# Kernel optimization log

Measured on AMD Instinct MI355X. Metric: run time of the kernel, lower is better.

The kernel has to match this reference:

```python
import jax, jax.numpy as jnp
import numpy as np
from jax import lax

D_MODEL = 512
EXPAND = 2
INNER = D_MODEL * EXPAND
K = 4
B, T = 8, 2048
LN_EPS = 1e-5


def setup_inputs() -> dict:
    key = jax.random.key(0)
    ks = jax.random.split(key, 12)
    s_in = 1.0 / np.sqrt(D_MODEL)
    s_out = 1.0 / np.sqrt(INNER)
    return {
        "x": jax.random.normal(ks[0], (B, T, D_MODEL), dtype=jnp.float32),
        "ln_w": jnp.ones((D_MODEL,), jnp.float32),
        "ln_b": jnp.zeros((D_MODEL,), jnp.float32),
        "in_proj_w": jax.random.uniform(ks[1], (3 * INNER, D_MODEL), jnp.float32, -s_in, s_in),
        "in_proj_b": jax.random.uniform(ks[2], (3 * INNER,), jnp.float32, -s_in, s_in),
        "conv_w": jax.random.uniform(ks[3], (INNER, 1, K), jnp.float32, -0.5, 0.5),
        "conv_b": jax.random.uniform(ks[4], (INNER,), jnp.float32, -0.5, 0.5),
        "delta_w": jax.random.uniform(ks[5], (INNER, D_MODEL), jnp.float32, -s_in, s_in),
        "delta_b": jax.random.uniform(ks[6], (INNER,), jnp.float32, -s_in, s_in),
        "state_mix": jnp.zeros((INNER,), jnp.float32),
        "skip_scale": jnp.ones((INNER,), jnp.float32),
        "out_proj_w": jax.random.uniform(ks[7], (D_MODEL, INNER), jnp.float32, -s_out, s_out),
        "out_proj_b": jax.random.uniform(ks[8], (D_MODEL,), jnp.float32, -s_out, s_out),
    }


def _layernorm(x, w, b):
    mu = jnp.mean(x, axis=-1, keepdims=True)
    var = jnp.mean(jnp.square(x - mu), axis=-1, keepdims=True)
    return (x - mu) * lax.rsqrt(var + LN_EPS) * w + b


def _causal_dw_conv(x_bct, w, b):
    # x: [B, C, T], w: [C, 1, K] depthwise, left pad K-1 (causal)
    y = lax.conv_general_dilated(
        x_bct, w, window_strides=(1,), padding=[(K - 1, 0)],
        dimension_numbers=("NCH", "OIH", "NCH"), feature_group_count=INNER)
    return y + b[None, :, None]


def reference(x, ln_w, ln_b, in_proj_w, in_proj_b, conv_w, conv_b,
              delta_w, delta_b, state_mix, skip_scale, out_proj_w, out_proj_b):
    residual = x
    xn = _layernorm(x, ln_w, ln_b)                      # [B,T,D]
    h = xn @ in_proj_w.T + in_proj_b                     # [B,T,3*INNER]
    proj, gate, drive = jnp.split(h, 3, axis=-1)
    proj = jax.nn.silu(proj)
    gate = jax.nn.sigmoid(gate)
    conv_out = _causal_dw_conv(jnp.swapaxes(proj, 1, 2), conv_w, conv_b)
    conv_out = jnp.swapaxes(conv_out, 1, 2)              # [B,T,INNER]
    delta = jnp.maximum(jax.nn.sigmoid(xn @ delta_w.T + delta_b), 1e-4)
    drive = jnp.tanh(drive)
    a = jax.nn.sigmoid(state_mix)                        # [INNER]
    d = delta * drive                                    # [B,T,INNER]

    def step(state, d_t):
        state = a * state + d_t
        return state, state

    _, states = lax.scan(step, jnp.zeros((x.shape[0], INNER), x.dtype),
                         jnp.swapaxes(d, 0, 1))          # [T,B,INNER]
    states = jnp.swapaxes(states, 0, 1)                  # [B,T,INNER]
    y = (states + skip_scale * conv_out) * gate
    y = y @ out_proj_w.T + out_proj_b
    return residual + y
```

## Files before the change

### kernel.cpp

```cpp
#include <hip/hip_runtime.h>
#include <stdint.h>

#define D_MODEL 512
#define INNER   1024
#define NCAT    4096
#define BATCH   8
#define SEQ     2048
#define ROWS    (BATCH*SEQ)
#define LN_EPS  1e-5f
#define CHUNK   64
#define NCHUNK  (SEQ/CHUNK)

typedef unsigned short u16;
typedef unsigned int   u32;
typedef __attribute__((ext_vector_type(8))) short bf16x8;
typedef __attribute__((ext_vector_type(4))) float f32x4;

__device__ __forceinline__ u16 f2bf(float f) {
  u32 u = __builtin_bit_cast(u32, f);
  return (u16)((u + 0x7FFFu + ((u >> 16) & 1u)) >> 16);
}
__device__ __forceinline__ float bf2f(u32 lo) {
  return __builtin_bit_cast(float, lo << 16);
}
__device__ __forceinline__ float sigf(float x){ return 1.f/(1.f+__expf(-x)); }

__device__ __forceinline__ void glds16(const void* g, void* l) {
  __builtin_amdgcn_global_load_lds((const __attribute__((address_space(1))) void*)g,
                                   (__attribute__((address_space(3))) void*)l, 16, 0, 0);
}

#define MFMA16(a,b,c) __builtin_amdgcn_mfma_f32_16x16x32_bf16((a),(b),(c),0,0,0)

__global__ __launch_bounds__(256) void prep_kernel(const float* __restrict__ x,
    const float* __restrict__ lw, const float* __restrict__ lb,
    const float* __restrict__ ipw, const float* __restrict__ dw,
    const float* __restrict__ opw, const float* __restrict__ ipb,
    const float* __restrict__ db, u16* __restrict__ xn,
    u16* __restrict__ wcat, u16* __restrict__ wout, float* __restrict__ bcat) {
  const int bid = blockIdx.x;
  if (bid < ROWS/4) {
    const int row  = bid * 4 + (threadIdx.x >> 6);
    const int lane = threadIdx.x & 63;
    const float4* xr = (const float4*)(x + (size_t)row * D_MODEL);
    float4 v0 = xr[lane*2], v1 = xr[lane*2+1];
    float s  = v0.x+v0.y+v0.z+v0.w + v1.x+v1.y+v1.z+v1.w;
    float s2 = v0.x*v0.x+v0.y*v0.y+v0.z*v0.z+v0.w*v0.w
             + v1.x*v1.x+v1.y*v1.y+v1.z*v1.z+v1.w*v1.w;
    #pragma unroll
    for (int o=32;o;o>>=1){ s += __shfl_xor(s,o); s2 += __shfl_xor(s2,o); }
    const float mu = s * (1.f/D_MODEL);
    const float rs = rsqrtf(s2*(1.f/D_MODEL) - mu*mu + LN_EPS);
    const float4* wv = (const float4*)lw; const float4* bv = (const float4*)lb;
    float4 w0 = wv[lane*2], w1 = wv[lane*2+1];
    float4 b0 = bv[lane*2], b1 = bv[lane*2+1];
    u32 p0 = (u32)f2bf((v0.x-mu)*rs*w0.x+b0.x) | ((u32)f2bf((v0.y-mu)*rs*w0.y+b0.y)<<16);
    u32 p1 = (u32)f2bf((v0.z-mu)*rs*w0.z+b0.z) | ((u32)f2bf((v0.w-mu)*rs*w0.w+b0.w)<<16);
    u32 p2 = (u32)f2bf((v1.x-mu)*rs*w1.x+b1.x) | ((u32)f2bf((v1.y-mu)*rs*w1.y+b1.y)<<16);
    u32 p3 = (u32)f2bf((v1.z-mu)*rs*w1.z+b1.z) | ((u32)f2bf((v1.w-mu)*rs*w1.w+b1.w)<<16);
    ((uint4*)(xn + (size_t)row * D_MODEL))[lane] = make_uint4(p0,p1,p2,p3);
  } else {
    const int i = (bid - ROWS/4)*256 + threadIdx.x;
    const int NW1 = NCAT*D_MODEL, NW2 = D_MODEL*INNER, STR = 1024*256;
    for (int idx = i; idx < NW1; idx += STR) {
      const int r = idx >> 9, c = idx & 511;
      float v;
      if (r < 2048) v = ipw[idx];
      else {
        const int rr = r - 2048;
        v = (rr & 1) ? dw[(size_t)(rr>>1)*D_MODEL + c]
                     : ipw[(size_t)(2048 + (rr>>1))*D_MODEL + c];
      }
      wcat[idx] = f2bf(v);
    }
    for (int idx = i; idx < NW2; idx += STR) wout[idx] = f2bf(opw[idx]);
    if (i < NCAT) {
      float b;
      if (i < 2048) b = ipb[i];
      else { const int rr = i - 2048; b = (rr & 1) ? db[rr>>1] : ipb[2048 + (rr>>1)]; }
      bcat[i] = b;
    }
  }
}

__device__ __forceinline__ void sched_blk(int nbm, int nbn, int GM, int GN,
                                          int& bM, int& bN) {
  const int nwg = nbm * nbn;
  const int bid = blockIdx.x;
  const int cpx = nwg >> 3;
  const int swz = (bid & 7) * cpx + (bid >> 3);
  const int gsz = GM * GN;
  const int g   = swz / gsz, loc = swz - g * gsz;
  const int ngn = nbn / GN;
  const int gm  = g / ngn,  gn  = g - gm * ngn;
  bM = gm * GM + (loc % GM);
  bN = gn * GN + (loc / GM);
}

__global__ __launch_bounds__(512, 2) void gemm1_kernel(const u16* __restrict__ A,
    const u16* __restrict__ Bm, const float* __restrict__ bcat,
    const float* __restrict__ sm, u16* __restrict__ proj, u16* __restrict__ gate,
    u16* __restrict__ dbuf, float* __restrict__ cS) {
  extern __shared__ u16 lds[];
  const int tid = threadIdx.x;
  int bM, bN; sched_blk(ROWS/256, NCAT/256, 8, 4, bM, bN);

  const u16* gA0; const u16* gA1; const u16* gB0; const u16* gB1;
  {
    const int p0 = tid,        q0 = p0>>3, t0 = (p0&7) ^ (q0&7);
    const int p1 = 512 + tid,  q1 = p1>>3, t1 = (p1&7) ^ (q1&7);
    const int rA0 = q0*2 + (t0>>2), sA0 = t0&3;
    const int rA1 = q1*2 + (t1>>2), sA1 = t1&3;
    gA0 = A + (size_t)(bM*256 + rA0)*D_MODEL + sA0*8;
    gA1 = A + (size_t)(bM*256 + rA1)*D_MODEL + sA1*8;
    const int c0 = (rA0 & ~63) + ((rA0&15)*4) + ((rA0>>4)&3);
    const int c1 = (rA1 & ~63) + ((rA1&15)*4) + ((rA1>>4)&3);
    gB0 = Bm + (size_t)(bN*256 + c0)*D_MODEL + sA0*8;
    gB1 = Bm + (size_t)(bN*256 + c1)*D_MODEL + sA1*8;
  }

#define STAGE1(KOFF, BUFO) do { \
    glds16(gA0 + (KOFF), lds + (BUFO) + tid*8); \
    glds16(gA1 + (KOFF), lds + (BUFO) + 4096 + tid*8); \
    glds16(gB0 + (KOFF), lds + (BUFO) + 8192 + tid*8); \
    glds16(gB1 + (KOFF), lds + (BUFO) + 12288 + tid*8); } while(0)

  const int lane = tid & 63, wid = tid >> 6;
  const int wm = wid >> 2, wn = wid & 3;
  const int rl = lane & 15;
  const int e  = (((lane&1)<<2) + (lane>>4)) ^ (rl>>1);
  const int aoff = wm*4096 + (rl>>1)*64 + e*8;
  const int boff = 8192 + wn*2048 + (rl>>1)*64 + e*8;

  f32x4 acc[8][4];
  #pragma unroll
  for (int m=0;m<8;m++)
    #pragma unroll
    for (int n=0;n<4;n++) acc[m][n] = (f32x4){0.f,0.f,0.f,0.f};

  STAGE1(0, 0);
  STAGE1(32, 16384);
  asm volatile("s_waitcnt vmcnt(4)" ::: "memory");
  __builtin_amdgcn_s_barrier();
  __builtin_amdgcn_sched_barrier(0);

  int cur = 0, stg = 32768;
  for (int kt = 0; kt < 16; ++kt) {
    bf16x8 af[8], bfr[4];
    #pragma unroll
    for (int m=0;m<8;m++) af[m]  = *(const bf16x8*)&lds[cur + aoff + m*512];
    #pragma unroll
    for (int n=0;n<4;n++) bfr[n] = *(const bf16x8*)&lds[cur + boff + n*512];
    if (kt + 2 < 16) STAGE1((kt+2)*32, stg);
    #pragma unroll
    for (int m=0;m<8;m++)
      #pragma unroll
      for (int n=0;n<4;n++)
        acc[m][n] = MFMA16(af[m], bfr[n], acc[m][n]);
    if (kt + 2 < 16) { asm volatile("s_waitcnt vmcnt(4)" ::: "memory"); }
    else             { asm volatile("s_waitcnt vmcnt(0)" ::: "memory"); }
    __builtin_amdgcn_s_barrier();
    __builtin_amdgcn_sched_barrier(0);
    cur += 16384; if (cur == 49152) cur = 0;
    stg += 16384; if (stg == 49152) stg = 0;
  }
#undef STAGE1

  const int colb = bN*256 + wn*64 + rl*4;
  const float4 b4 = *(const float4*)&bcat[colb];
  const float* bp = (const float*)&b4;
  if (colb < 2048) {
    u16* outp = (colb < 1024) ? proj : gate;
    const int lcolb = colb & (INNER-1);
    #pragma unroll
    for (int m=0;m<8;m++) {
      const int row0 = bM*256 + wm*128 + m*16 + ((lane>>4)<<2);
      #pragma unroll
      for (int r=0;r<4;r++) {
        float a4[4];
        #pragma unroll
        for (int n=0;n<4;n++) {
          float v = acc[m][n][r] + bp[n];
          a4[n] = (colb < 1024) ? v * sigf(v) : sigf(v);
        }
        u32 lo = (u32)f2bf(a4[0]) | ((u32)f2bf(a4[1])<<16);
        u32 hi = (u32)f2bf(a4[2]) | ((u32)f2bf(a4[3])<<16);
        *(uint2*)&outp[(size_t)(row0+r)*INNER + lcolb] = make_uint2(lo, hi);
      }
    }
  } else {
    const int ch0 = (colb - 2048) >> 1;
    const int g = lane >> 4;
    const float A0 = sigf(sm[ch0]), A1 = sigf(sm[ch0+1]);
    const float A0_2 = A0*A0,   A1_2 = A1*A1;
    const float A0_4 = A0_2*A0_2, A1_4 = A1_2*A1_2;
    const float A0_8 = A0_4*A0_4, A1_8 = A1_4*A1_4;
    const float A0_16 = A0_8*A0_8, A1_16 = A1_8*A1_8;
    float S0a = 0.f, S0b = 0.f, S1a = 0.f, S1b = 0.f;
    #pragma unroll
    for (int m=0;m<8;m++) {
      const int row0 = bM*256 + wm*128 + m*16 + (g<<2);
      float sg0 = 0.f, sg1 = 0.f;
      #pragma unroll
      for (int r=0;r<4;r++) {
        const float v0 = acc[m][0][r] + bp[0];
        const float v1 = acc[m][1][r] + bp[1];
        const float v2 = acc[m][2][r] + bp[2];
        const float v3 = acc[m][3][r] + bp[3];
        const float d0 = (2.f*sigf(2.f*v0) - 1.f) * fmaxf(sigf(v1), 1e-4f);
        const float d1 = (2.f*sigf(2.f*v2) - 1.f) * fmaxf(sigf(v3), 1e-4f);
        *(u32*)&dbuf[(size_t)(row0+r)*INNER + ch0] = (u32)f2bf(d0) | ((u32)f2bf(d1)<<16);
        sg0 = A0*sg0 + d0;
        sg1 = A1*sg1 + d1;
      }
      float p0 = __shfl_xor(sg0, 16), p1 = __shfl_xor(sg1, 16);
      float e0 = (g & 1) ? (sg0 + A0_4*p0) : (p0 + A0_4*sg0);
      float e1 = (g & 1) ? (sg1 + A1_4*p1) : (p1 + A1_4*sg1);
      float q0 = __shfl_xor(e0, 32), q1 = __shfl_xor(e1, 32);
      float s16_0 = (g & 2) ? (e0 + A0_8*q0) : (q0 + A0_8*e0);
      float s16_1 = (g & 2) ? (e1 + A1_8*q1) : (q1 + A1_8*e1);
      if (m < 4) { S0a = A0_16*S0a + s16_0; S1a = A1_16*S1a + s16_1; }
      else       { S0b = A0_16*S0b + s16_0; S1b = A1_16*S1b + s16_1; }
    }
    if (g == 0) {
      const int b = bM >> 3;
      const int chunk0 = (bM & 7)*4 + wm*2;
      const size_t o0 = ((size_t)b*NCHUNK + chunk0    )*INNER + ch0;
      const size_t o1 = ((size_t)b*NCHUNK + chunk0 + 1)*INNER + ch0;
      *(float2*)&cS[o0] = make_float2(S0a, S1a);
      *(float2*)&cS[o1] = make_float2(S0b, S1b);
    }
  }
}

__device__ __forceinline__ void gemm_main(const u16* __restrict__ A,
    const u16* __restrict__ Bm, int K, int nkt, int bM, int bN,
    u16* lA, u16* lB, f32x4 acc[4][4]) {
  const int tid = threadIdx.x;
  const int l6  = tid >> 2;
  const int sg  = (tid & 3) ^ (l6 & 3);
  const int pB  = (l6 & 15) * 4 + ((l6 >> 4) & 3);
  const u16* gA = A  + (size_t)(bM*128 + l6)*K + sg*8;
  const u16* gB = Bm + (size_t)(bN*128 + pB)*K + sg*8;
  u16* dA = lA + tid*8;
  u16* dB = lB + tid*8;
  const size_t rstep = (size_t)64*K;

#define STAGE_T(koff, bufo) do { \
    const u16* sA = gA + (koff); const u16* sB = gB + (koff); \
    glds16(sA,         dA + (bufo));        glds16(sA + rstep, dA + (bufo) + 2048); \
    glds16(sB,         dB + (bufo));        glds16(sB + rstep, dB + (bufo) + 2048); \
  } while (0)

  STAGE_T(0, 0);
  STAGE_T(32, 4096);
  asm volatile("s_waitcnt vmcnt(4)" ::: "memory");
  __builtin_amdgcn_s_barrier();
  __builtin_amdgcn_sched_barrier(0);

  const int lane = tid & 63, wv = tid >> 6;
  const int wm = wv >> 1, wn = wv & 1;
  const int kx = ((lane>>4) ^ (lane&3)) * 8;
  const int aoff = (wm*64 + (lane&15))*32 + kx;
  const int boff = (wn*64 + (lane&15))*32 + kx;

  int cur = 0, stg = 8192;
  for (int kt = 0; kt < nkt; ++kt) {
    bf16x8 af[4], bfr[4];
    #pragma unroll
    for (int m=0;m<4;m++) af[m]  = *(const bf16x8*)&lA[cur + aoff + m*512];
    #pragma unroll
    for (int n=0;n<4;n++) bfr[n] = *(const bf16x8*)&lB[cur + boff + n*512];
    if (kt + 2 < nkt) STAGE_T((kt+2)*32, stg);
    #pragma unroll
    for (int m=0;m<4;m++)
      #pragma unroll
      for (int n=0;n<4;n++)
        acc[m][n] = MFMA16(af[m], bfr[n], acc[m][n]);
    if (kt + 2 < nkt) { asm volatile("s_waitcnt vmcnt(4)" ::: "memory"); }
    else              { asm volatile("s_waitcnt vmcnt(0)" ::: "memory"); }
    __builtin_amdgcn_s_barrier();
    __builtin_amdgcn_sched_barrier(0);
    cur += 4096; if (cur == 12288) cur = 0;
    stg += 4096; if (stg == 12288) stg = 0;
  }
#undef STAGE_T
}

__global__ __launch_bounds__(256, 3) void gemm2_kernel(const u16* __restrict__ A,
    const u16* __restrict__ Bm, const float* __restrict__ ob,
    const float* __restrict__ resid, float* __restrict__ out) {
  __shared__ u16 lA[12288], lB[12288];
  f32x4 acc[4][4];
  #pragma unroll
  for (int m=0;m<4;m++)
    #pragma unroll
    for (int n=0;n<4;n++) acc[m][n] = (f32x4){0.f,0.f,0.f,0.f};
  int bM, bN; sched_blk(ROWS/128, D_MODEL/128, 8, 4, bM, bN);
  gemm_main(A, Bm, INNER, INNER/32, bM, bN, lA, lB, acc);
  const int lane = threadIdx.x & 63, wv = threadIdx.x >> 6;
  const int wm = wv>>1, wn = wv&1;
  const int colb = bN*128 + wn*64 + (lane&15)*4;
  const float4 ob4 = *(const float4*)&ob[colb];
  #pragma unroll
  for (int m=0;m<4;m++) {
    const int row0 = bM*128 + wm*64 + m*16 + ((lane>>4)<<2);
    #pragma unroll
    for (int r=0;r<4;r++) {
      const size_t idx = (size_t)(row0+r)*D_MODEL + colb;
      float4 rs = *(const float4*)&resid[idx];
      float4 o;
      o.x = acc[m][0][r] + ob4.x + rs.x;
      o.y = acc[m][1][r] + ob4.y + rs.y;
      o.z = acc[m][2][r] + ob4.z + rs.z;
      o.w = acc[m][3][r] + ob4.w + rs.w;
      *(float4*)&out[idx] = o;
    }
  }
}

__global__ __launch_bounds__(256) void scan3_kernel(const u16* __restrict__ proj,
    const u16* __restrict__ gate, const u16* __restrict__ d,
    const float* __restrict__ cS, const float* __restrict__ sm,
    const float* __restrict__ cw, const float* __restrict__ cb,
    const float* __restrict__ sk, u16* __restrict__ z) {
  const int blk = blockIdx.x;
  const int half = blk & 1, ch = (blk>>1) & (NCHUNK-1), b = blk >> 6;
  const int c0 = half*512 + threadIdx.x*2;
  const float a0 = sigf(sm[c0]), a1 = sigf(sm[c0+1]);
  const float cb0 = cb[c0], cb1 = cb[c0+1];
  const float sk0 = sk[c0], sk1 = sk[c0+1];
  const float w00=cw[c0*4+0], w01=cw[c0*4+1], w02=cw[c0*4+2], w03=cw[c0*4+3];
  const float w10=cw[c0*4+4], w11=cw[c0*4+5], w12=cw[c0*4+6], w13=cw[c0*4+7];
  float A0 = a0, A1 = a1;
  #pragma unroll
  for (int i=0;i<6;i++){ A0*=A0; A1*=A1; }
  float s0 = 0.f, s1 = 0.f;
  for (int j = 0; j < ch; ++j) {
    const size_t oj = ((size_t)b*NCHUNK + j)*INNER + c0;
    const float2 cv = *(const float2*)&cS[oj];
    s0 = A0*s0 + cv.x;
    s1 = A1*s1 + cv.y;
  }
  const int t0 = ch*CHUNK;
  const size_t rowb = (size_t)b*SEQ*INNER + c0;
  float pa0=0,pb0=0,pc0=0, pa1=0,pb1=0,pc1=0;
  if (ch > 0) {
    u32 u3 = *(const u32*)(proj + rowb + (size_t)(t0-3)*INNER);
    u32 u2 = *(const u32*)(proj + rowb + (size_t)(t0-2)*INNER);
    u32 u1 = *(const u32*)(proj + rowb + (size_t)(t0-1)*INNER);
    pa0 = bf2f(u3&0xffffu); pa1 = bf2f(u3>>16);
    pb0 = bf2f(u2&0xffffu); pb1 = bf2f(u2>>16);
    pc0 = bf2f(u1&0xffffu); pc1 = bf2f(u1>>16);
  }
  size_t base = rowb + (size_t)t0*INNER;
  for (int t=0;t<CHUNK;t++) {
    u32 pu = *(const u32*)(proj + base);
    const float pd0 = bf2f(pu&0xffffu), pd1 = bf2f(pu>>16);
    const float co0 = w00*pa0 + w01*pb0 + w02*pc0 + w03*pd0 + cb0;
    const float co1 = w10*pa1 + w11*pb1 + w12*pc1 + w13*pd1 + cb1;
    pa0=pb0; pb0=pc0; pc0=pd0;  pa1=pb1; pb1=pc1; pc1=pd1;
    u32 du = *(const u32*)(d + base);
    s0 = a0*s0 + bf2f(du&0xffffu);
    s1 = a1*s1 + bf2f(du>>16);
    u32 gu = *(const u32*)(gate + base);
    const float z0 = (s0 + sk0*co0)*bf2f(gu&0xffffu);
    const float z1 = (s1 + sk1*co1)*bf2f(gu>>16);
    *(u32*)(z + base) = (u32)f2bf(z0) | ((u32)f2bf(z1)<<16);
    base += INNER;
  }
}

extern "C" void kernel_launch(void* const* d_in, const int* in_sizes, int n_in,
                              void* d_out, int out_size, void* d_ws, size_t ws_size,
                              hipStream_t stream) {
  const float* x    = (const float*)d_in[0];
  const float* ln_w = (const float*)d_in[1];
  const float* ln_b = (const float*)d_in[2];
  const float* ipw  = (const float*)d_in[3];
  const float* ipb  = (const float*)d_in[4];
  const float* cw   = (const float*)d_in[5];
  const float* cb   = (const float*)d_in[6];
  const float* dw   = (const float*)d_in[7];
  const float* db   = (const float*)d_in[8];
  const float* sm   = (const float*)d_in[9];
  const float* sk   = (const float*)d_in[10];
  const float* opw  = (const float*)d_in[11];
  const float* opb  = (const float*)d_in[12];
  float* out = (float*)d_out;

  uint8_t* w = (uint8_t*)d_ws;
  u16* xn    = (u16*)w;  w += (size_t)ROWS*D_MODEL*2;
  u16* wcat  = (u16*)w;  w += (size_t)NCAT*D_MODEL*2;
  u16* wout  = (u16*)w;  w += (size_t)D_MODEL*INNER*2;
  u16* proj  = (u16*)w;  w += (size_t)ROWS*INNER*2;
  u16* gate  = (u16*)w;  w += (size_t)ROWS*INNER*2;
  u16* dbuf  = (u16*)w;  w += (size_t)ROWS*INNER*2;
  u16* z     = (u16*)w;  w += (size_t)ROWS*INNER*2;
  float* cS    = (float*)w; w += (size_t)BATCH*NCHUNK*INNER*4;
  float* bcat  = (float*)w; w += (size_t)NCAT*4;

  prep_kernel<<<ROWS/4 + 1024, 256, 0, stream>>>(x, ln_w, ln_b, ipw, dw, opw, ipb, db,
                                                 xn, wcat, wout, bcat);
  gemm1_kernel<<<(ROWS/256)*(NCAT/256), 512, 98304, stream>>>(xn, wcat, bcat, sm, proj, gate, dbuf, cS);
  scan3_kernel<<<BATCH*NCHUNK*2, 256, 0, stream>>>(proj, gate, dbuf, cS, sm, cw, cb, sk, z);
  gemm2_kernel<<<(ROWS/128)*(D_MODEL/128), 256, 0, stream>>>(z, wout, opb, x, out);
}
```

Measured before the change: 166.0 us.

## Restructure GEMM1 main loop to four-buffer ring with two k-tiles per barrier

The GEMM1 K-loop moves from a 3-stage LDS ring with one barrier per k-tile to a 4-buffer ring. Each iteration stages two k-tiles ahead and computes two, so barriers and vmcnt waits are halved. Dynamic LDS grows from 96KB to 128KB, and the loop now waits for all outstanding loads (vmcnt(0)) before each barrier. That can expose global latency, and the larger LDS footprint may limit occupancy.

```diff
diff --git a/kernel.cpp b/kernel.cpp
--- a/kernel.cpp
+++ b/kernel.cpp
@@ -140,29 +140,46 @@
 
   STAGE1(0, 0);
   STAGE1(32, 16384);
-  asm volatile("s_waitcnt vmcnt(4)" ::: "memory");
+  asm volatile("s_waitcnt vmcnt(0)" ::: "memory");
   __builtin_amdgcn_s_barrier();
   __builtin_amdgcn_sched_barrier(0);
 
-  int cur = 0, stg = 32768;
-  for (int kt = 0; kt < 16; ++kt) {
-    bf16x8 af[8], bfr[4];
-    #pragma unroll
-    for (int m=0;m<8;m++) af[m]  = *(const bf16x8*)&lds[cur + aoff + m*512];
-    #pragma unroll
-    for (int n=0;n<4;n++) bfr[n] = *(const bf16x8*)&lds[cur + boff + n*512];
-    if (kt + 2 < 16) STAGE1((kt+2)*32, stg);
-    #pragma unroll
-    for (int m=0;m<8;m++)
-      #pragma unroll
-      for (int n=0;n<4;n++)
-        acc[m][n] = MFMA16(af[m], bfr[n], acc[m][n]);
-    if (kt + 2 < 16) { asm volatile("s_waitcnt vmcnt(4)" ::: "memory"); }
-    else             { asm volatile("s_waitcnt vmcnt(0)" ::: "memory"); }
+  #pragma unroll
+  for (int s = 0; s < 8; ++s) {
+    const int te = 2*s;
+    const int be = (te & 3) << 14;
+    const int bo = ((te+1) & 3) << 14;
+    if (s < 7) {
+      STAGE1((te+2)*32, ((te+2) & 3) << 14);
+      STAGE1((te+3)*32, ((te+3) & 3) << 14);
+    }
+    {
+      bf16x8 af[8], bfr[4];
+      #pragma unroll
+      for (int m=0;m<8;m++) af[m]  = *(const bf16x8*)&lds[be + aoff + m*512];
+      #pragma unroll
+      for (int n=0;n<4;n++) bfr[n] = *(const bf16x8*)&lds[be + boff + n*512];
+      #pragma unroll
+      for (int m=0;m<8;m++)
+        #pragma unroll
+        for (int n=0;n<4;n++)
+          acc[m][n] = MFMA16(af[m], bfr[n], acc[m][n]);
+    }
+    {
+      bf16x8 af[8], bfr[4];
+      #pragma unroll
+      for (int m=0;m<8;m++) af[m]  = *(const bf16x8*)&lds[bo + aoff + m*512];
+      #pragma unroll
+      for (int n=0;n<4;n++) bfr[n] = *(const bf16x8*)&lds[bo + boff + n*512];
+      #pragma unroll
+      for (int m=0;m<8;m++)
+        #pragma unroll
+        for (int n=0;n<4;n++)
+          acc[m][n] = MFMA16(af[m], bfr[n], acc[m][n]);
+    }
+    asm volatile("s_waitcnt vmcnt(0)" ::: "memory");
     __builtin_amdgcn_s_barrier();
     __builtin_amdgcn_sched_barrier(0);
-    cur += 16384; if (cur == 49152) cur = 0;
-    stg += 16384; if (stg == 49152) stg = 0;
   }
 #undef STAGE1
 
@@ -402,7 +419,7 @@
 
   prep_kernel<<<ROWS/4 + 1024, 256, 0, stream>>>(x, ln_w, ln_b, ipw, dw, opw, ipb, db,
                                                  xn, wcat, wout, bcat);
-  gemm1_kernel<<<(ROWS/256)*(NCAT/256), 512, 98304, stream>>>(xn, wcat, bcat, sm, proj, gate, dbuf, cS);
+  gemm1_kernel<<<(ROWS/256)*(NCAT/256), 512, 131072, stream>>>(xn, wcat, bcat, sm, proj, gate, dbuf, cS);
   scan3_kernel<<<BATCH*NCHUNK*2, 256, 0, stream>>>(proj, gate, dbuf, cS, sm, cw, cb, sk, z);
   gemm2_kernel<<<(ROWS/128)*(D_MODEL/128), 256, 0, stream>>>(z, wout, opb, x, out);
 }
```

Result: no change. 167.5 us (+0.9%).

## Fuse scan/gating stage with output projection GEMM via LDS-resident z tile

Applied to the files above, without the earlier changes.

Merges the scan3 kernel and the output-projection GEMM into one kernel. Each block computes the gated scan output z for a 64-row chunk across all 1024 channels into a 128KB swizzled LDS buffer, then runs the 64x512 GEMM against wout directly from LDS, adding bias and residual. This removes the round trip of z through global memory and one launch. In exchange the grid shrinks to 256 blocks with one block per CU, the wout fragments are read straight from global/L2 without LDS staging, and the epilogue stores become scalar instead of float4.

```diff
diff --git a/kernel.cpp b/kernel.cpp
--- a/kernel.cpp
+++ b/kernel.cpp
@@ -233,141 +233,110 @@
   }
 }
 
-__device__ __forceinline__ void gemm_main(const u16* __restrict__ A,
-    const u16* __restrict__ Bm, int K, int nkt, int bM, int bN,
-    u16* lA, u16* lB, f32x4 acc[4][4]) {
+__global__ __launch_bounds__(512, 1) void fused_sg2_kernel(const u16* __restrict__ proj,
+    const u16* __restrict__ gate, const u16* __restrict__ d,
+    const float* __restrict__ cS, const float* __restrict__ sm,
+    const float* __restrict__ cw, const float* __restrict__ cb,
+    const float* __restrict__ sk, const u16* __restrict__ wout,
+    const float* __restrict__ ob, const float* __restrict__ resid,
+    float* __restrict__ out) {
+  extern __shared__ u16 zl[];
   const int tid = threadIdx.x;
-  const int l6  = tid >> 2;
-  const int sg  = (tid & 3) ^ (l6 & 3);
-  const int pB  = (l6 & 15) * 4 + ((l6 >> 4) & 3);
-  const u16* gA = A  + (size_t)(bM*128 + l6)*K + sg*8;
-  const u16* gB = Bm + (size_t)(bN*128 + pB)*K + sg*8;
-  u16* dA = lA + tid*8;
-  u16* dB = lB + tid*8;
-  const size_t rstep = (size_t)64*K;
-
-#define STAGE_T(koff, bufo) do { \
-    const u16* sA = gA + (koff); const u16* sB = gB + (koff); \
-    glds16(sA,         dA + (bufo));        glds16(sA + rstep, dA + (bufo) + 2048); \
-    glds16(sB,         dB + (bufo));        glds16(sB + rstep, dB + (bufo) + 2048); \
-  } while (0)
-
-  STAGE_T(0, 0);
-  STAGE_T(32, 4096);
-  asm volatile("s_waitcnt vmcnt(4)" ::: "memory");
-  __builtin_amdgcn_s_barrier();
-  __builtin_amdgcn_sched_barrier(0);
-
-  const int lane = tid & 63, wv = tid >> 6;
-  const int wm = wv >> 1, wn = wv & 1;
-  const int kx = ((lane>>4) ^ (lane&3)) * 8;
-  const int aoff = (wm*64 + (lane&15))*32 + kx;
-  const int boff = (wn*64 + (lane&15))*32 + kx;
-
-  int cur = 0, stg = 8192;
-  for (int kt = 0; kt < nkt; ++kt) {
-    bf16x8 af[4], bfr[4];
-    #pragma unroll
-    for (int m=0;m<4;m++) af[m]  = *(const bf16x8*)&lA[cur + aoff + m*512];
-    #pragma unroll
-    for (int n=0;n<4;n++) bfr[n] = *(const bf16x8*)&lB[cur + boff + n*512];
-    if (kt + 2 < nkt) STAGE_T((kt+2)*32, stg);
-    #pragma unroll
-    for (int m=0;m<4;m++)
-      #pragma unroll
-      for (int n=0;n<4;n++)
-        acc[m][n] = MFMA16(af[m], bfr[n], acc[m][n]);
-    if (kt + 2 < nkt) { asm volatile("s_waitcnt vmcnt(4)" ::: "memory"); }
-    else              { asm volatile("s_waitcnt vmcnt(0)" ::: "memory"); }
-    __builtin_amdgcn_s_barrier();
-    __builtin_amdgcn_sched_barrier(0);
-    cur += 4096; if (cur == 12288) cur = 0;
-    stg += 4096; if (stg == 12288) stg = 0;
-  }
-#undef STAGE_T
-}
-
-__global__ __launch_bounds__(256, 3) void gemm2_kernel(const u16* __restrict__ A,
-    const u16* __restrict__ Bm, const float* __restrict__ ob,
-    const float* __restrict__ resid, float* __restrict__ out) {
-  __shared__ u16 lA[12288], lB[12288];
+  const int b = blockIdx.x >> 5, ch = blockIdx.x & 31;
+  const int t0 = ch*CHUNK;
+
+  {
+    const int c0 = tid*2;
+    const float a0 = sigf(sm[c0]), a1 = sigf(sm[c0+1]);
+    const float cb0 = cb[c0], cb1 = cb[c0+1];
+    const float sk0 = sk[c0], sk1 = sk[c0+1];
+    const float w00=cw[c0*4+0], w01=cw[c0*4+1], w02=cw[c0*4+2], w03=cw[c0*4+3];
+    const float w10=cw[c0*4+4], w11=cw[c0*4+5], w12=cw[c0*4+6], w13=cw[c0*4+7];
+    float A0 = a0, A1 = a1;
+    #pragma unroll
+    for (int i=0;i<6;i++){ A0*=A0; A1*=A1; }
+    float s0 = 0.f, s1 = 0.f;
+    for (int j = 0; j < ch; ++j) {
+      const size_t oj = ((size_t)b*NCHUNK + j)*INNER + c0;
+      const float2 cv = *(const float2*)&cS[oj];
+      s0 = A0*s0 + cv.x;
+      s1 = A1*s1 + cv.y;
+    }
+    const size_t rowb = (size_t)b*SEQ*INNER + c0;
+    float pa0=0,pb0=0,pc0=0, pa1=0,pb1=0,pc1=0;
+    if (ch > 0) {
+      u32 u3 = *(const u32*)(proj + rowb + (size_t)(t0-3)*INNER);
+      u32 u2 = *(const u32*)(proj + rowb + (size_t)(t0-2)*INNER);
+      u32 u1 = *(const u32*)(proj + rowb + (size_t)(t0-1)*INNER);
+      pa0 = bf2f(u3&0xffffu); pa1 = bf2f(u3>>16);
+      pb0 = bf2f(u2&0xffffu); pb1 = bf2f(u2>>16);
+      pc0 = bf2f(u1&0xffffu); pc1 = bf2f(u1>>16);
+    }
+    const int ck = c0 >> 3, wi = c0 & 7;
+    size_t base = rowb + (size_t)t0*INNER;
+    for (int t=0;t<CHUNK;t++) {
+      u32 pu = *(const u32*)(proj + base);
+      const float pd0 = bf2f(pu&0xffffu), pd1 = bf2f(pu>>16);
+      const float co0 = w00*pa0 + w01*pb0 + w02*pc0 + w03*pd0 + cb0;
+      const float co1 = w10*pa1 + w11*pb1 + w12*pc1 + w13*pd1 + cb1;
+      pa0=pb0; pb0=pc0; pc0=pd0;  pa1=pb1; pb1=pc1; pc1=pd1;
+      u32 du = *(const u32*)(d + base);
+      s0 = a0*s0 + bf2f(du&0xffffu);
+      s1 = a1*s1 + bf2f(du>>16);
+      u32 gu = *(const u32*)(gate + base);
+      const float z0 = (s0 + sk0*co0)*bf2f(gu&0xffffu);
+      const float z1 = (s1 + sk1*co1)*bf2f(gu>>16);
+      const int zi = t*1024 + (((ck ^ (t&7)) << 3) | wi);
+      *(u32*)&zl[zi] = (u32)f2bf(z0) | ((u32)f2bf(z1)<<16);
+      base += INNER;
+    }
+  }
+  __syncthreads();
+
+  const int lane = tid & 63, w8 = tid >> 6;
+  const int nb0 = w8*64;
+  const int r15 = lane & 15, k8 = lane >> 4;
   f32x4 acc[4][4];
   #pragma unroll
   for (int m=0;m<4;m++)
     #pragma unroll
     for (int n=0;n<4;n++) acc[m][n] = (f32x4){0.f,0.f,0.f,0.f};
-  int bM, bN; sched_blk(ROWS/128, D_MODEL/128, 8, 4, bM, bN);
-  gemm_main(A, Bm, INNER, INNER/32, bM, bN, lA, lB, acc);
-  const int lane = threadIdx.x & 63, wv = threadIdx.x >> 6;
-  const int wm = wv>>1, wn = wv&1;
-  const int colb = bN*128 + wn*64 + (lane&15)*4;
-  const float4 ob4 = *(const float4*)&ob[colb];
+
+  const u16* gB = wout + (size_t)(nb0 + r15)*INNER + k8*8;
+
+  #pragma unroll 4
+  for (int kk = 0; kk < 32; ++kk) {
+    bf16x8 bfr[4];
+    #pragma unroll
+    for (int n=0;n<4;n++)
+      bfr[n] = *(const bf16x8*)(gB + (size_t)(n*16)*INNER + kk*32);
+    bf16x8 afr[4];
+    #pragma unroll
+    for (int m=0;m<4;m++) {
+      const int row = m*16 + r15;
+      const int lchunk = kk*4 + k8;
+      afr[m] = *(const bf16x8*)&zl[row*1024 + ((lchunk ^ (row&7)) << 3)];
+    }
+    #pragma unroll
+    for (int m=0;m<4;m++)
+      #pragma unroll
+      for (int n=0;n<4;n++)
+        acc[m][n] = MFMA16(afr[m], bfr[n], acc[m][n]);
+  }
+
   #pragma unroll
-  for (int m=0;m<4;m++) {
-    const int row0 = bM*128 + wm*64 + m*16 + ((lane>>4)<<2);
-    #pragma unroll
-    for (int r=0;r<4;r++) {
-      const size_t idx = (size_t)(row0+r)*D_MODEL + colb;
-      float4 rs = *(const float4*)&resid[idx];
-      float4 o;
-      o.x = acc[m][0][r] + ob4.x + rs.x;
-      o.y = acc[m][1][r] + ob4.y + rs.y;
-      o.z = acc[m][2][r] + ob4.z + rs.z;
-      o.w = acc[m][3][r] + ob4.w + rs.w;
-      *(float4*)&out[idx] = o;
-    }
-  }
-}
-
-__global__ __launch_bounds__(256) void scan3_kernel(const u16* __restrict__ proj,
-    const u16* __restrict__ gate, const u16* __restrict__ d,
-    const float* __restrict__ cS, const float* __restrict__ sm,
-    const float* __restrict__ cw, const float* __restrict__ cb,
-    const float* __restrict__ sk, u16* __restrict__ z) {
-  const int blk = blockIdx.x;
-  const int half = blk & 1, ch = (blk>>1) & (NCHUNK-1), b = blk >> 6;
-  const int c0 = half*512 + threadIdx.x*2;
-  const float a0 = sigf(sm[c0]), a1 = sigf(sm[c0+1]);
-  const float cb0 = cb[c0], cb1 = cb[c0+1];
-  const float sk0 = sk[c0], sk1 = sk[c0+1];
-  const float w00=cw[c0*4+0], w01=cw[c0*4+1], w02=cw[c0*4+2], w03=cw[c0*4+3];
-  const float w10=cw[c0*4+4], w11=cw[c0*4+5], w12=cw[c0*4+6], w13=cw[c0*4+7];
-  float A0 = a0, A1 = a1;
-  #pragma unroll
-  for (int i=0;i<6;i++){ A0*=A0; A1*=A1; }
-  float s0 = 0.f, s1 = 0.f;
-  for (int j = 0; j < ch; ++j) {
-    const size_t oj = ((size_t)b*NCHUNK + j)*INNER + c0;
-    const float2 cv = *(const float2*)&cS[oj];
-    s0 = A0*s0 + cv.x;
-    s1 = A1*s1 + cv.y;
-  }
-  const int t0 = ch*CHUNK;
-  const size_t rowb = (size_t)b*SEQ*INNER + c0;
-  float pa0=0,pb0=0,pc0=0, pa1=0,pb1=0,pc1=0;
-  if (ch > 0) {
-    u32 u3 = *(const u32*)(proj + rowb + (size_t)(t0-3)*INNER);
-    u32 u2 = *(const u32*)(proj + rowb + (size_t)(t0-2)*INNER);
-    u32 u1 = *(const u32*)(proj + rowb + (size_t)(t0-1)*INNER);
-    pa0 = bf2f(u3&0xffffu); pa1 = bf2f(u3>>16);
-    pb0 = bf2f(u2&0xffffu); pb1 = bf2f(u2>>16);
-    pc0 = bf2f(u1&0xffffu); pc1 = bf2f(u1>>16);
-  }
-  size_t base = rowb + (size_t)t0*INNER;
-  for (int t=0;t<CHUNK;t++) {
-    u32 pu = *(const u32*)(proj + base);
-    const float pd0 = bf2f(pu&0xffffu), pd1 = bf2f(pu>>16);
-    const float co0 = w00*pa0 + w01*pb0 + w02*pc0 + w03*pd0 + cb0;
-    const float co1 = w10*pa1 + w11*pb1 + w12*pc1 + w13*pd1 + cb1;
-    pa0=pb0; pb0=pc0; pc0=pd0;  pa1=pb1; pb1=pc1; pc1=pd1;
-    u32 du = *(const u32*)(d + base);
-    s0 = a0*s0 + bf2f(du&0xffffu);
-    s1 = a1*s1 + bf2f(du>>16);
-    u32 gu = *(const u32*)(gate + base);
-    const float z0 = (s0 + sk0*co0)*bf2f(gu&0xffffu);
-    const float z1 = (s1 + sk1*co1)*bf2f(gu>>16);
-    *(u32*)(z + base) = (u32)f2bf(z0) | ((u32)f2bf(z1)<<16);
-    base += INNER;
+  for (int n=0;n<4;n++) {
+    const int col = nb0 + n*16 + r15;
+    const float bias = ob[col];
+    #pragma unroll
+    for (int m=0;m<4;m++) {
+      const int grow = b*SEQ + t0 + m*16 + (k8<<2);
+      #pragma unroll
+      for (int r=0;r<4;r++) {
+        const size_t idx = (size_t)(grow + r)*D_MODEL + col;
+        out[idx] = acc[m][n][r] + bias + resid[idx];
+      }
+    }
   }
 }
 
@@ -396,13 +365,12 @@
   u16* proj  = (u16*)w;  w += (size_t)ROWS*INNER*2;
   u16* gate  = (u16*)w;  w += (size_t)ROWS*INNER*2;
   u16* dbuf  = (u16*)w;  w += (size_t)ROWS*INNER*2;
-  u16* z     = (u16*)w;  w += (size_t)ROWS*INNER*2;
   float* cS    = (float*)w; w += (size_t)BATCH*NCHUNK*INNER*4;
   float* bcat  = (float*)w; w += (size_t)NCAT*4;
 
   prep_kernel<<<ROWS/4 + 1024, 256, 0, stream>>>(x, ln_w, ln_b, ipw, dw, opw, ipb, db,
                                                  xn, wcat, wout, bcat);
   gemm1_kernel<<<(ROWS/256)*(NCAT/256), 512, 98304, stream>>>(xn, wcat, bcat, sm, proj, gate, dbuf, cS);
-  scan3_kernel<<<BATCH*NCHUNK*2, 256, 0, stream>>>(proj, gate, dbuf, cS, sm, cw, cb, sk, z);
-  gemm2_kernel<<<(ROWS/128)*(D_MODEL/128), 256, 0, stream>>>(z, wout, opb, x, out);
-}
+  fused_sg2_kernel<<<BATCH*NCHUNK, 512, 131072, stream>>>(proj, gate, dbuf, cS, sm, cw, cb,
+                                                          sk, wout, opb, x, out);
+}
```

Measured after the change: 171.7 us. +3.4%, slower.
